# Kernel optimization log

Hardware: AMD Instinct MI355X
Metric: run time of the kernel (lower is better)

## Reference

```python
import jax, jax.numpy as jnp
import numpy as np

NEG_INF = -1e9  # stands in for the eye(W)*sys.maxsize self-mask on the row axis


def setup_inputs() -> dict:
    key = jax.random.key(0)
    ks = jax.random.split(key, 8)
    B, C, S = 8, 512, 128
    C8 = C // 8
    sc = 0.02
    x = jax.random.normal(ks[0], (B, C, S, S), dtype=jnp.float32)
    Wq = jax.random.normal(ks[1], (C8, C), dtype=jnp.float32) * sc
    bq = jnp.zeros((C8,), dtype=jnp.float32)
    Wk = jax.random.normal(ks[2], (C8, C), dtype=jnp.float32) * sc
    bk = jnp.zeros((C8,), dtype=jnp.float32)
    Wv = jax.random.normal(ks[3], (C, C), dtype=jnp.float32) * sc
    bv = jnp.zeros((C,), dtype=jnp.float32)
    gamma = jnp.ones((1,), dtype=jnp.float32) * 0.5  # source inits to 0; nonzero so path is exercised
    return {"x": x, "Wq": Wq, "bq": bq, "Wk": Wk, "bk": bk, "Wv": Wv, "bv": bv, "gamma": gamma}


def reference(x, Wq, bq, Wk, bk, Wv, bv, gamma):
    # x: (B, C, W, H) with W == H == S (required by the eye-mask view in the source)
    B, C, S, _ = x.shape
    # 1x1 convs = per-pixel linear projections
    q = jnp.einsum('oc,bcwh->bowh', Wq, x) + bq[None, :, None, None]  # (B,C8,S,S)
    k = jnp.einsum('oc,bcwh->bowh', Wk, x) + bk[None, :, None, None]
    v = jnp.einsum('oc,bcwh->bowh', Wv, x) + bv[None, :, None, None]  # (B,C,S,S)

    # column ('h'-fixed) attention along W, self position masked out
    e_col = jnp.einsum('bcwh,bcuh->bwhu', q, k)  # (B,W,H,W)
    self_mask = jnp.eye(S, dtype=bool)  # w == u
    e_col = jnp.where(self_mask[None, :, None, :], NEG_INF, e_col)
    # row ('w'-fixed) attention along H
    e_row = jnp.einsum('bcwh,bcwu->bwhu', q, k)  # (B,W,H,H)

    att = jax.nn.softmax(jnp.concatenate([e_col, e_row], axis=-1), axis=-1)  # (B,W,H,2S)
    a_col = att[..., :S]   # weights over w'
    a_row = att[..., S:]   # weights over h'

    out = (jnp.einsum('bwhu,bcuh->bcwh', a_col, v)
           + jnp.einsum('bwhu,bcwu->bcwh', a_row, v))  # (B,C,S,S)
    return gamma[0] * out + x
```

## Files before the change

### kernel.cpp

```cpp
#include <hip/hip_runtime.h>
#include <hip/hip_bf16.h>


#define S 128
#define SS 16384
#define C 512
#define C8 64
#define NEG_BIG -1000000000.0f

using short8 = __attribute__((ext_vector_type(8))) short;
using f32x4  = __attribute__((ext_vector_type(4))) float;

#define GPTR(p) ((const __attribute__((address_space(1))) void*)(p))
#define LPTR(p) ((__attribute__((address_space(3))) void*)(p))

#define PR(r) ((((r) & 7) << 4) | ((r) >> 3))

__device__ __forceinline__ unsigned short f2b(float f){
  union { float f; unsigned u; } v; v.f = f;
  unsigned r = (v.u + 0x7fffu + ((v.u >> 16) & 1u)) >> 16;
  return (unsigned short)r;
}
__device__ __forceinline__ float b2f(unsigned short h){
  union { unsigned u; float f; } v; v.u = ((unsigned)h) << 16;
  return v.f;
}

template<int NT>
__device__ __forceinline__ void stage_tile64(unsigned short* dst,
    const unsigned short* src, size_t rstride, int tid){
  #pragma unroll
  for (int p = 0; p < 1024 / NT; ++p){
    int gi = p * NT + tid;
    int row = gi >> 3, cc = gi & 7;
    int kc = (cc ^ (row & 7)) * 8;
    __builtin_amdgcn_global_load_lds(GPTR(src + (size_t)row * rstride + kc),
                                     LPTR((char*)dst + gi * 16), 16, 0, 0);
  }
}

__global__ __launch_bounds__(256) void k_xp_pack(
    const float* __restrict__ x, unsigned short* __restrict__ xp,
    const float* __restrict__ Wq, const float* __restrict__ Wk,
    const float* __restrict__ Wv, unsigned short* __restrict__ wall){
  __shared__ unsigned short T[128 * 130] __attribute__((aligned(16)));
  int blk = blockIdx.x;
  if (blk >= 4096){
    int i = (blk - 4096) * 256 + threadIdx.x;
    int co = i >> 9, ci = i & (C - 1);
    float v;
    if (co < 64)        v = Wq[co * C + ci];
    else if (co < 128)  v = Wk[(co - 64) * C + ci];
    else                v = Wv[(co - 128) * C + ci];
    wall[i] = f2b(v);
    return;
  }
  int ct = blk & 3; int bw = blk >> 2;
  int w = bw & 127; int b = bw >> 7;
  int tid = threadIdx.x;
  int ci0 = ct * 128;
  const float* xb = x + ((size_t)(b * C + ci0) * S + w) * S;
  #pragma unroll
  for (int p = 0; p < 16; ++p){
    int idx = p * 256 + tid;
    int cc = idx >> 5;
    int h4 = (idx & 31) * 4;
    float4 v = *(const float4*)(xb + (size_t)cc * SS + h4);
    unsigned* d = (unsigned*)&T[PR(cc) * 130 + h4];
    d[0] = (unsigned)f2b(v.x) | ((unsigned)f2b(v.y) << 16);
    d[1] = (unsigned)f2b(v.z) | ((unsigned)f2b(v.w) << 16);
  }
  __syncthreads();
  unsigned short* xpb = xp + (size_t)(b * S + w) * S * C + ci0;
  #pragma unroll
  for (int p = 0; p < 8; ++p){
    int idx = p * 256 + tid;
    int h  = idx >> 4;
    int ch = (idx & 15) * 8;
    unsigned short tmp[8] __attribute__((aligned(16)));
    #pragma unroll
    for (int j = 0; j < 8; ++j) tmp[j] = T[PR(ch + j) * 130 + h];
    *(uint4*)(xpb + (size_t)h * C + ch) = *(uint4*)tmp;
  }
}

__global__ __launch_bounds__(512) void k_qkv(
    const unsigned short* __restrict__ xp, const unsigned short* __restrict__ wall,
    const float* __restrict__ bq, const float* __restrict__ bk,
    const float* __restrict__ bv,
    unsigned short* __restrict__ qp, unsigned short* __restrict__ kp,
    unsigned short* __restrict__ vb){
  __shared__ unsigned short sm[32768] __attribute__((aligned(16)));
  unsigned short* Dl = sm;
  int blk = blockIdx.x;
  int pxsub = blk & 7; int t = blk >> 3;
  int cot = t % 5; int pxg = t / 5;
  int pxt = pxg * 8 + pxsub;
  int w = pxt & 127, b = pxt >> 7;
  int tid = threadIdx.x, lane = tid & 63, wid = tid >> 6;
  int wr = wid & 1, wc = wid >> 1;
  int qd = lane >> 4, ln = lane & 15;
  const unsigned short* asrc0 = wall + (size_t)cot * 128 * C;
  const unsigned short* bsrc0 = xp + (size_t)pxt * 128 * C;
  f32x4 acc[4][2];
  #pragma unroll
  for (int i = 0; i < 4; ++i)
    #pragma unroll
    for (int j = 0; j < 2; ++j) acc[i][j] = (f32x4){0.f, 0.f, 0.f, 0.f};

  stage_tile64<512>(sm,        asrc0, C, tid);
  stage_tile64<512>(sm + 8192, bsrc0, C, tid);
  __syncthreads();

  for (int kw = 0; kw < 8; ++kw){
    unsigned short* Acur = sm + (kw & 1) * 16384;
    unsigned short* Bcur = Acur + 8192;
    if (kw < 7){
      unsigned short* Anxt = sm + ((kw + 1) & 1) * 16384;
      stage_tile64<512>(Anxt,        asrc0 + (kw + 1) * 64, C, tid);
      stage_tile64<512>(Anxt + 8192, bsrc0 + (kw + 1) * 64, C, tid);
    }
    __builtin_amdgcn_s_setprio(1);
    #pragma unroll
    for (int ks = 0; ks < 2; ++ks){
      int ch8 = (((ks * 4 + qd) ^ (ln & 7)) * 8);
      short8 af[4], bfr[2];
      #pragma unroll
      for (int i = 0; i < 4; ++i)
        af[i] = *(const short8*)&Acur[((wr * 4 + i) * 16 + ln) * 64 + ch8];
      #pragma unroll
      for (int j = 0; j < 2; ++j)
        bfr[j] = *(const short8*)&Bcur[((wc * 2 + j) * 16 + ln) * 64 + ch8];
      #pragma unroll
      for (int i = 0; i < 4; ++i)
        #pragma unroll
        for (int j = 0; j < 2; ++j)
          acc[i][j] = __builtin_amdgcn_mfma_f32_16x16x32_bf16(af[i], bfr[j], acc[i][j], 0, 0, 0);
    }
    __builtin_amdgcn_s_setprio(0);
    __syncthreads();
  }
  float bias_[4][4];
  #pragma unroll
  for (int i = 0; i < 4; ++i){
    int co_l0 = (wr * 4 + i) * 16 + qd * 4;
    #pragma unroll
    for (int r = 0; r < 4; ++r){
      int co_l = co_l0 + r;
      bias_[i][r] = (cot == 0) ? (co_l < 64 ? bq[co_l] : bk[co_l - 64])
                               : bv[(cot - 1) * 128 + co_l];
    }
  }
  #pragma unroll
  for (int i = 0; i < 4; ++i){
    int co_l0 = (wr * 4 + i) * 16 + qd * 4;
    #pragma unroll
    for (int j = 0; j < 2; ++j){
      int pxl = (wc * 2 + j) * 16 + ln;
      #pragma unroll
      for (int r = 0; r < 4; ++r)
        Dl[(co_l0 + r) * 136 + pxl] = f2b(acc[i][j][r] + bias_[i][r]);
    }
  }
  __syncthreads();
  if (cot == 0){
    unsigned short* qb = qp + (size_t)(b * S + w) * S * C8;
    unsigned short* kb = kp + (size_t)(b * S + w) * S * C8;
    #pragma unroll
    for (int p = 0; p < 2; ++p){
      int idx = p * 512 + tid;
      int cch = idx & 7, hh = idx >> 3;
      unsigned short tq[8] __attribute__((aligned(16)));
      unsigned short tk[8] __attribute__((aligned(16)));
      #pragma unroll
      for (int jj = 0; jj < 8; ++jj){
        tq[jj] = Dl[(cch * 8 + jj) * 136 + hh];
        tk[jj] = Dl[(64 + cch * 8 + jj) * 136 + hh];
      }
      *(uint4*)(qb + (size_t)hh * C8 + cch * 8) = *(uint4*)tq;
      *(uint4*)(kb + (size_t)hh * C8 + cch * 8) = *(uint4*)tk;
    }
  } else {
    unsigned short* vbb = vb + ((size_t)(b * C + (cot - 1) * 128) * S + w) * S;
    #pragma unroll
    for (int p = 0; p < 4; ++p){
      int idx = p * 512 + tid;
      int c_l = idx >> 4, hc = (idx & 15) * 8;
      uint4 v = *(const uint4*)&Dl[c_l * 136 + hc];
      *(uint4*)(vbb + (size_t)c_l * SS + hc) = v;
    }
  }
}

__global__ __launch_bounds__(256) void k_tv_ecol(
    const unsigned short* __restrict__ vb, unsigned short* __restrict__ vt,
    const unsigned short* __restrict__ qp, const unsigned short* __restrict__ kp,
    unsigned short* __restrict__ eca){
  __shared__ char smu[36864] __attribute__((aligned(16)));
  int blk = blockIdx.x;
  int tid = threadIdx.x;
  if (blk < 4096){
    unsigned short* T = (unsigned short*)smu;
    const unsigned short* src = vb + (size_t)blk * SS;
    unsigned short* dst = vt + (size_t)blk * SS;
    #pragma unroll
    for (int p = 0; p < 8; ++p){
      int idx = p * 256 + tid;
      int wv = idx >> 4, ch = (idx & 15) * 8;
      uint4 v = *(const uint4*)(src + wv * S + ch);
      unsigned* d = (unsigned*)&T[PR(wv) * 130 + ch];
      d[0] = v.x; d[1] = v.y; d[2] = v.z; d[3] = v.w;
    }
    __syncthreads();
    #pragma unroll
    for (int p = 0; p < 8; ++p){
      int idx = p * 256 + tid;
      int h = idx >> 4, ch = (idx & 15) * 8;
      unsigned short tmp[8] __attribute__((aligned(16)));
      #pragma unroll
      for (int j = 0; j < 8; ++j) tmp[j] = T[PR(ch + j) * 130 + h];
      *(uint4*)(dst + h * S + ch) = *(uint4*)tmp;
    }
    return;
  }
  unsigned short* Aq = (unsigned short*)smu;
  unsigned short* Bk = (unsigned short*)(smu + 18432);
  int e = blk - 4096; int h = e & 127, b = e >> 7;
  int lane = tid & 63, wid = tid >> 6;
  int qd = lane >> 4, ln = lane & 15;
  #pragma unroll
  for (int p = 0; p < 4; ++p){
    int idx = p * 256 + tid;
    int row = idx >> 3, ch = (idx & 7) * 8;
    *(uint4*)&Aq[row * 72 + ch] = *(const uint4*)(qp + ((size_t)(b * S + row) * S + h) * C8 + ch);
    *(uint4*)&Bk[row * 72 + ch] = *(const uint4*)(kp + ((size_t)(b * S + row) * S + h) * C8 + ch);
  }
  __syncthreads();
  f32x4 acc[4][4];
  #pragma unroll
  for (int i = 0; i < 4; ++i)
    #pragma unroll
    for (int j = 0; j < 4; ++j) acc[i][j] = (f32x4){0.f, 0.f, 0.f, 0.f};
  #pragma unroll
  for (int ks = 0; ks < 2; ++ks){
    int ko = ks * 32 + qd * 8;
    short8 af[4], bfr[4];
    #pragma unroll
    for (int i = 0; i < 4; ++i)
      af[i] = *(const short8*)&Aq[(((wid & 1) * 4 + i) * 16 + ln) * 72 + ko];
    #pragma unroll
    for (int j = 0; j < 4; ++j)
      bfr[j] = *(const short8*)&Bk[(((wid >> 1) * 4 + j) * 16 + ln) * 72 + ko];
    #pragma unroll
    for (int i = 0; i < 4; ++i)
      #pragma unroll
      for (int j = 0; j < 4; ++j)
        acc[i][j] = __builtin_amdgcn_mfma_f32_16x16x32_bf16(af[i], bfr[j], acc[i][j], 0, 0, 0);
  }
  #pragma unroll
  for (int i = 0; i < 4; ++i){
    int w0 = (((wid & 1) * 4 + i) * 16) + qd * 4;
    #pragma unroll
    for (int j = 0; j < 4; ++j){
      int ug = ((wid >> 1) * 4 + j) * 16 + ln;
      #pragma unroll
      for (int r = 0; r < 4; ++r){
        int wg = w0 + r;
        float val = acc[i][j][r];
        if (wg == ug) val = NEG_BIG;
        eca[((size_t)(b * S + wg) * S + h) * S + ug] = f2b(val);
      }
    }
  }
}

__global__ __launch_bounds__(256) void k_erow_sm_outrow(
    const unsigned short* __restrict__ qp, const unsigned short* __restrict__ kp,
    unsigned short* __restrict__ eca, unsigned short* vb){
  __shared__ char sm[71680] __attribute__((aligned(16)));
  unsigned short* Aq  = (unsigned short*)sm;
  unsigned short* Bk  = (unsigned short*)(sm + 18432);
  unsigned short* El  = (unsigned short*)sm;
  unsigned short* Av0 = (unsigned short*)(sm + 36864);
  unsigned short* Av1 = (unsigned short*)(sm + 53248);
  float* redm = (float*)(sm + 69632);
  float* reds = (float*)(sm + 70656);
  int blk = blockIdx.x; int w = blk & 127, b = blk >> 7;
  int tid = threadIdx.x, lane = tid & 63, wid = tid >> 6;
  int qd = lane >> 4, ln = lane & 15;
  size_t tb = (size_t)(b * S + w) * SS;
  const unsigned short* vsrc0 = vb + (size_t)(b * C) * SS + (size_t)w * S;

  {
    const unsigned short* qsrc = qp + (size_t)(b * S + w) * S * C8;
    const unsigned short* ksrc = kp + (size_t)(b * S + w) * S * C8;
    #pragma unroll
    for (int p = 0; p < 4; ++p){
      int idx = p * 256 + tid;
      int row = idx >> 3, ch = (idx & 7) * 8;
      *(uint4*)&Aq[row * 72 + ch] = *(const uint4*)(qsrc + row * C8 + ch);
      *(uint4*)&Bk[row * 72 + ch] = *(const uint4*)(ksrc + row * C8 + ch);
    }
  }
  stage_tile64<256>(Av0, vsrc0, SS, tid);
  __syncthreads();
  f32x4 acc[4][4];
  #pragma unroll
  for (int i = 0; i < 4; ++i)
    #pragma unroll
    for (int j = 0; j < 4; ++j) acc[i][j] = (f32x4){0.f, 0.f, 0.f, 0.f};
  #pragma unroll
  for (int ks = 0; ks < 2; ++ks){
    int ko = ks * 32 + qd * 8;
    short8 af[4], bfr[4];
    #pragma unroll
    for (int i = 0; i < 4; ++i)
      af[i] = *(const short8*)&Aq[(((wid & 1) * 4 + i) * 16 + ln) * 72 + ko];
    #pragma unroll
    for (int j = 0; j < 4; ++j)
      bfr[j] = *(const short8*)&Bk[(((wid >> 1) * 4 + j) * 16 + ln) * 72 + ko];
    #pragma unroll
    for (int i = 0; i < 4; ++i)
      #pragma unroll
      for (int j = 0; j < 4; ++j)
        acc[i][j] = __builtin_amdgcn_mfma_f32_16x16x32_bf16(af[i], bfr[j], acc[i][j], 0, 0, 0);
  }
  __syncthreads();
  #pragma unroll
  for (int i = 0; i < 4; ++i){
    int h0 = ((wid & 1) * 4 + i) * 16 + qd * 4;
    #pragma unroll
    for (int j = 0; j < 4; ++j){
      int ul = ((wid >> 1) * 4 + j) * 16 + ln;
      #pragma unroll
      for (int r = 0; r < 4; ++r)
        El[(h0 + r) * 136 + ul] = f2b(acc[i][j][r]);
    }
  }
  __syncthreads();
  {
    int h = tid >> 1, half = tid & 1;
    const uint4* src4 = (half == 0) ? (const uint4*)(eca + tb + (size_t)h * S)
                                    : (const uint4*)&El[h * 136];
    float mx = -3.0e38f;
    #pragma unroll 4
    for (int u = 0; u < 16; ++u){
      uint4 v = src4[u];
      const unsigned short* e = (const unsigned short*)&v;
      #pragma unroll
      for (int jj = 0; jj < 8; ++jj) mx = fmaxf(mx, b2f(e[jj]));
    }
    redm[tid] = mx;
    __syncthreads();
    float m = fmaxf(mx, redm[tid ^ 1]);
    float s = 0.f;
    #pragma unroll 4
    for (int u = 0; u < 16; ++u){
      uint4 v = src4[u];
      const unsigned short* e = (const unsigned short*)&v;
      #pragma unroll
      for (int jj = 0; jj < 8; ++jj) s += __expf(b2f(e[jj]) - m);
    }
    reds[tid] = s;
    __syncthreads();
    float inv = 1.0f / (s + reds[tid ^ 1]);
    uint4* dst4 = (half == 0) ? (uint4*)(eca + tb + (size_t)h * S)
                              : (uint4*)&El[h * 136];
    #pragma unroll 4
    for (int u = 0; u < 16; ++u){
      uint4 v = src4[u];
      const unsigned short* e = (const unsigned short*)&v;
      unsigned short o[8] __attribute__((aligned(16)));
      #pragma unroll
      for (int jj = 0; jj < 8; ++jj) o[jj] = f2b(__expf(b2f(e[jj]) - m) * inv);
      dst4[u] = *(uint4*)o;
    }
  }
  __syncthreads();

  for (int s = 0; s < 8; ++s){
    int ct = s >> 1, kw = s & 1;
    unsigned short* Acur = (s & 1) ? Av1 : Av0;
    if (s < 7){
      int ct1 = (s + 1) >> 1, kw1 = (s + 1) & 1;
      stage_tile64<256>((s & 1) ? Av0 : Av1,
                        vsrc0 + (size_t)(ct1 * 128) * SS + kw1 * 64, SS, tid);
    }
    if (kw == 0){
      #pragma unroll
      for (int i = 0; i < 4; ++i)
        #pragma unroll
        for (int j = 0; j < 4; ++j) acc[i][j] = (f32x4){0.f, 0.f, 0.f, 0.f};
    }
    __builtin_amdgcn_s_setprio(1);
    #pragma unroll
    for (int ks = 0; ks < 2; ++ks){
      int ch8 = (((ks * 4 + qd) ^ (ln & 7)) * 8);
      int ko = kw * 64 + ks * 32 + qd * 8;
      short8 af[4], bfr[4];
      #pragma unroll
      for (int i = 0; i < 4; ++i)
        af[i] = *(const short8*)&Acur[(((wid & 1) * 4 + i) * 16 + ln) * 64 + ch8];
      #pragma unroll
      for (int j = 0; j < 4; ++j)
        bfr[j] = *(const short8*)&El[(((wid >> 1) * 4 + j) * 16 + ln) * 136 + ko];
      #pragma unroll
      for (int i = 0; i < 4; ++i)
        #pragma unroll
        for (int j = 0; j < 4; ++j)
          acc[i][j] = __builtin_amdgcn_mfma_f32_16x16x32_bf16(af[i], bfr[j], acc[i][j], 0, 0, 0);
    }
    __builtin_amdgcn_s_setprio(0);
    if (kw == 1){
      #pragma unroll
      for (int i = 0; i < 4; ++i){
        int c0 = ((wid & 1) * 4 + i) * 16 + qd * 4;
        #pragma unroll
        for (int j = 0; j < 4; ++j){
          int hl = ((wid >> 1) * 4 + j) * 16 + ln;
          #pragma unroll
          for (int r = 0; r < 4; ++r){
            int cg = ct * 128 + c0 + r;
            vb[((size_t)(b * C + cg) * S + w) * S + hl] = f2b(acc[i][j][r]);
          }
        }
      }
    }
    __syncthreads();
  }
}

__global__ __launch_bounds__(256) void k_outcol(
    const unsigned short* __restrict__ vt, const unsigned short* __restrict__ eca,
    unsigned short* __restrict__ oct){
  __shared__ unsigned short Av[128 * 72] __attribute__((aligned(16)));
  __shared__ unsigned short Ba[128 * 72] __attribute__((aligned(16)));
  int blk = blockIdx.x;
  int ct = blk & 3; int bh = blk >> 2;
  int h = bh & 127, b = bh >> 7;
  int tid = threadIdx.x, lane = tid & 63, wid = tid >> 6;
  int qd = lane >> 4, ln = lane & 15;
  f32x4 acc[4][4];
  #pragma unroll
  for (int i = 0; i < 4; ++i)
    #pragma unroll
    for (int j = 0; j < 4; ++j) acc[i][j] = (f32x4){0.f, 0.f, 0.f, 0.f};
  for (int kw = 0; kw < 2; ++kw){
    __syncthreads();
    #pragma unroll
    for (int p = 0; p < 4; ++p){
      int idx = p * 256 + tid;
      int row = idx >> 3, ch = (idx & 7) * 8;
      *(uint4*)&Av[row * 72 + ch] =
        *(const uint4*)(vt + ((size_t)(b * C + ct * 128 + row) * S + h) * S + kw * 64 + ch);
      *(uint4*)&Ba[row * 72 + ch] =
        *(const uint4*)(eca + ((size_t)(b * S + row) * S + h) * S + kw * 64 + ch);
    }
    __syncthreads();
    #pragma unroll
    for (int ks = 0; ks < 2; ++ks){
      int ko = ks * 32 + qd * 8;
      short8 af[4], bfr[4];
      #pragma unroll
      for (int i = 0; i < 4; ++i)
        af[i] = *(const short8*)&Av[(((wid & 1) * 4 + i) * 16 + ln) * 72 + ko];
      #pragma unroll
      for (int j = 0; j < 4; ++j)
        bfr[j] = *(const short8*)&Ba[(((wid >> 1) * 4 + j) * 16 + ln) * 72 + ko];
      #pragma unroll
      for (int i = 0; i < 4; ++i)
        #pragma unroll
        for (int j = 0; j < 4; ++j)
          acc[i][j] = __builtin_amdgcn_mfma_f32_16x16x32_bf16(af[i], bfr[j], acc[i][j], 0, 0, 0);
    }
  }
  #pragma unroll
  for (int i = 0; i < 4; ++i){
    int c0 = ((wid & 1) * 4 + i) * 16 + qd * 4;
    #pragma unroll
    for (int j = 0; j < 4; ++j){
      int wl = ((wid >> 1) * 4 + j) * 16 + ln;
      #pragma unroll
      for (int r = 0; r < 4; ++r){
        int cg = ct * 128 + c0 + r;
        oct[((size_t)(b * S + h) * C + cg) * S + wl] = f2b(acc[i][j][r]);
      }
    }
  }
}

__global__ __launch_bounds__(256) void k_final(
    const unsigned short* __restrict__ oct, const unsigned short* __restrict__ orw,
    const float* __restrict__ x, const float* __restrict__ gamma,
    float* __restrict__ out){
  __shared__ unsigned short T[128 * 130] __attribute__((aligned(16)));
  int blk = blockIdx.x;
  int c = blk & 511, b = blk >> 9;
  int tid = threadIdx.x;
  float g = gamma[0];
  #pragma unroll
  for (int p = 0; p < 8; ++p){
    int idx = p * 256 + tid;
    int hh = idx >> 4, ch = (idx & 15) * 8;
    uint4 v = *(const uint4*)(oct + ((size_t)(b * S + hh) * C + c) * S + ch);
    unsigned* d = (unsigned*)&T[PR(hh) * 130 + ch];
    d[0] = v.x; d[1] = v.y; d[2] = v.z; d[3] = v.w;
  }
  __syncthreads();
  #pragma unroll
  for (int p = 0; p < 8; ++p){
    int idx = p * 256 + tid;
    int wv = idx >> 4, hch = (idx & 15) * 8;
    size_t o = ((size_t)(b * C + c) * S + wv) * S + hch;
    uint4 rv = *(const uint4*)(orw + o);
    const unsigned short* rr = (const unsigned short*)&rv;
    float4 x0 = *(const float4*)(x + o);
    float4 x1 = *(const float4*)(x + o + 4);
    float4 o0, o1;
    o0.x = g * (b2f(rr[0]) + b2f(T[PR(hch + 0) * 130 + wv])) + x0.x;
    o0.y = g * (b2f(rr[1]) + b2f(T[PR(hch + 1) * 130 + wv])) + x0.y;
    o0.z = g * (b2f(rr[2]) + b2f(T[PR(hch + 2) * 130 + wv])) + x0.z;
    o0.w = g * (b2f(rr[3]) + b2f(T[PR(hch + 3) * 130 + wv])) + x0.w;
    o1.x = g * (b2f(rr[4]) + b2f(T[PR(hch + 4) * 130 + wv])) + x1.x;
    o1.y = g * (b2f(rr[5]) + b2f(T[PR(hch + 5) * 130 + wv])) + x1.y;
    o1.z = g * (b2f(rr[6]) + b2f(T[PR(hch + 6) * 130 + wv])) + x1.z;
    o1.w = g * (b2f(rr[7]) + b2f(T[PR(hch + 7) * 130 + wv])) + x1.w;
    *(float4*)(out + o) = o0;
    *(float4*)(out + o + 4) = o1;
  }
}

extern "C" void kernel_launch(void* const* d_in, const int* in_sizes, int n_in,
                              void* d_out, int out_size, void* d_ws, size_t ws_size,
                              hipStream_t stream){
  const float* x     = (const float*)d_in[0];
  const float* Wq    = (const float*)d_in[1];
  const float* bq    = (const float*)d_in[2];
  const float* Wk    = (const float*)d_in[3];
  const float* bk    = (const float*)d_in[4];
  const float* Wv    = (const float*)d_in[5];
  const float* bv    = (const float*)d_in[6];
  const float* gamma = (const float*)d_in[7];
  float* out = (float*)d_out;
  char* ws = (char*)d_ws;

  const size_t OFF_WALL = 0;
  const size_t OFF_XP   = 1ull << 20;
  const size_t OFF_QP   = OFF_XP  + 134217728ull;
  const size_t OFF_KP   = OFF_QP  + 16777216ull;
  const size_t OFF_VB   = OFF_KP  + 16777216ull;
  const size_t OFF_VT   = OFF_VB  + 134217728ull;
  const size_t OFF_ECA  = OFF_VT  + 134217728ull;
  const size_t OFF_OCT  = OFF_XP;
  const size_t NEED     = OFF_ECA + 33554432ull;
  if (ws_size < NEED) return;

  unsigned short* wall = (unsigned short*)(ws + OFF_WALL);
  unsigned short* xp   = (unsigned short*)(ws + OFF_XP);
  unsigned short* qp   = (unsigned short*)(ws + OFF_QP);
  unsigned short* kp   = (unsigned short*)(ws + OFF_KP);
  unsigned short* vb   = (unsigned short*)(ws + OFF_VB);
  unsigned short* vt   = (unsigned short*)(ws + OFF_VT);
  unsigned short* eca  = (unsigned short*)(ws + OFF_ECA);
  unsigned short* oct  = (unsigned short*)(ws + OFF_OCT);

  k_xp_pack       <<<5376, 256, 0, stream>>>(x, xp, Wq, Wk, Wv, wall);
  k_qkv           <<<5120, 512, 0, stream>>>(xp, wall, bq, bk, bv, qp, kp, vb);
  k_tv_ecol       <<<5120, 256, 0, stream>>>(vb, vt, qp, kp, eca);
  k_erow_sm_outrow<<<1024, 256, 0, stream>>>(qp, kp, eca, vb);
  k_outcol        <<<4096, 256, 0, stream>>>(vt, eca, oct);
  k_final         <<<4096, 256, 0, stream>>>(oct, vb, x, gamma, out);
}
```

Measured before the change: 917.3 us.

## Restructure QKV GEMM: weights in registers, triple-buffered LDS for activations

The QKV projection kernel drops from 512 to 256 threads per block, with each wave computing a 4x4 MFMA tile instead of 4x2. Weight fragments are now loaded from global memory directly into double-buffered registers, so only the activation tile goes through shared memory. That tile uses a three-slot LDS ring with prefetch two steps ahead, and explicit vmcnt waits plus a raw barrier replace the per-iteration __syncthreads. The aim is to cut LDS traffic and barrier stalls and to overlap loads with MFMA work. The cost is higher register pressure and fragile hand-counted waitcnt values.

Measured after the change: 990.2 us. +7.9%, slower.

```diff
diff --git a/kernel.cpp b/kernel.cpp
--- a/kernel.cpp
+++ b/kernel.cpp
@@ -84,13 +84,13 @@
   }
 }
 
-__global__ __launch_bounds__(512) void k_qkv(
+__global__ __launch_bounds__(256) void k_qkv(
     const unsigned short* __restrict__ xp, const unsigned short* __restrict__ wall,
     const float* __restrict__ bq, const float* __restrict__ bk,
     const float* __restrict__ bv,
     unsigned short* __restrict__ qp, unsigned short* __restrict__ kp,
     unsigned short* __restrict__ vb){
-  __shared__ unsigned short sm[32768] __attribute__((aligned(16)));
+  __shared__ unsigned short sm[24576] __attribute__((aligned(16)));
   unsigned short* Dl = sm;
   int blk = blockIdx.x;
   int pxsub = blk & 7; int t = blk >> 3;
@@ -98,52 +98,66 @@
   int pxt = pxg * 8 + pxsub;
   int w = pxt & 127, b = pxt >> 7;
   int tid = threadIdx.x, lane = tid & 63, wid = tid >> 6;
-  int wr = wid & 1, wc = wid >> 1;
   int qd = lane >> 4, ln = lane & 15;
   const unsigned short* asrc0 = wall + (size_t)cot * 128 * C;
   const unsigned short* bsrc0 = xp + (size_t)pxt * 128 * C;
-  f32x4 acc[4][2];
+  const unsigned short* arow[4];
   #pragma unroll
   for (int i = 0; i < 4; ++i)
-    #pragma unroll
-    for (int j = 0; j < 2; ++j) acc[i][j] = (f32x4){0.f, 0.f, 0.f, 0.f};
-
-  stage_tile64<512>(sm,        asrc0, C, tid);
-  stage_tile64<512>(sm + 8192, bsrc0, C, tid);
-  __syncthreads();
-
+    arow[i] = asrc0 + (size_t)(((wid & 1) * 4 + i) * 16 + ln) * C + qd * 8;
+  f32x4 acc[4][4];
+  #pragma unroll
+  for (int i = 0; i < 4; ++i)
+    #pragma unroll
+    for (int j = 0; j < 4; ++j) acc[i][j] = (f32x4){0.f, 0.f, 0.f, 0.f};
+  short8 afr[2][2][4];
+
+  stage_tile64<256>(sm,        bsrc0,      C, tid);
+  stage_tile64<256>(sm + 8192, bsrc0 + 64, C, tid);
+  #pragma unroll
+  for (int ks = 0; ks < 2; ++ks)
+    #pragma unroll
+    for (int i = 0; i < 4; ++i)
+      afr[0][ks][i] = *(const short8*)(arow[i] + ks * 32);
+
+  #pragma unroll
   for (int kw = 0; kw < 8; ++kw){
-    unsigned short* Acur = sm + (kw & 1) * 16384;
-    unsigned short* Bcur = Acur + 8192;
+    if (kw < 7) asm volatile("s_waitcnt vmcnt(12)" ::: "memory");
+    else        asm volatile("s_waitcnt vmcnt(0)"  ::: "memory");
+    __builtin_amdgcn_s_barrier();
     if (kw < 7){
-      unsigned short* Anxt = sm + ((kw + 1) & 1) * 16384;
-      stage_tile64<512>(Anxt,        asrc0 + (kw + 1) * 64, C, tid);
-      stage_tile64<512>(Anxt + 8192, bsrc0 + (kw + 1) * 64, C, tid);
-    }
+      #pragma unroll
+      for (int ks = 0; ks < 2; ++ks)
+        #pragma unroll
+        for (int i = 0; i < 4; ++i)
+          afr[(kw + 1) & 1][ks][i] =
+            *(const short8*)(arow[i] + (kw + 1) * 64 + ks * 32);
+    }
+    if (kw < 6)
+      stage_tile64<256>(sm + ((kw + 2) % 3) * 8192,
+                        bsrc0 + (kw + 2) * 64, C, tid);
+    const unsigned short* Bl = sm + (kw % 3) * 8192;
     __builtin_amdgcn_s_setprio(1);
     #pragma unroll
     for (int ks = 0; ks < 2; ++ks){
       int ch8 = (((ks * 4 + qd) ^ (ln & 7)) * 8);
-      short8 af[4], bfr[2];
-      #pragma unroll
-      for (int i = 0; i < 4; ++i)
-        af[i] = *(const short8*)&Acur[((wr * 4 + i) * 16 + ln) * 64 + ch8];
-      #pragma unroll
-      for (int j = 0; j < 2; ++j)
-        bfr[j] = *(const short8*)&Bcur[((wc * 2 + j) * 16 + ln) * 64 + ch8];
+      short8 bfr[4];
+      #pragma unroll
+      for (int j = 0; j < 4; ++j)
+        bfr[j] = *(const short8*)&Bl[(((wid >> 1) * 4 + j) * 16 + ln) * 64 + ch8];
       #pragma unroll
       for (int i = 0; i < 4; ++i)
         #pragma unroll
-        for (int j = 0; j < 2; ++j)
-          acc[i][j] = __builtin_amdgcn_mfma_f32_16x16x32_bf16(af[i], bfr[j], acc[i][j], 0, 0, 0);
+        for (int j = 0; j < 4; ++j)
+          acc[i][j] = __builtin_amdgcn_mfma_f32_16x16x32_bf16(afr[kw & 1][ks][i], bfr[j], acc[i][j], 0, 0, 0);
     }
     __builtin_amdgcn_s_setprio(0);
-    __syncthreads();
-  }
+  }
+  __syncthreads();
   float bias_[4][4];
   #pragma unroll
   for (int i = 0; i < 4; ++i){
-    int co_l0 = (wr * 4 + i) * 16 + qd * 4;
+    int co_l0 = ((wid & 1) * 4 + i) * 16 + qd * 4;
     #pragma unroll
     for (int r = 0; r < 4; ++r){
       int co_l = co_l0 + r;
@@ -153,10 +167,10 @@
   }
   #pragma unroll
   for (int i = 0; i < 4; ++i){
-    int co_l0 = (wr * 4 + i) * 16 + qd * 4;
-    #pragma unroll
-    for (int j = 0; j < 2; ++j){
-      int pxl = (wc * 2 + j) * 16 + ln;
+    int co_l0 = ((wid & 1) * 4 + i) * 16 + qd * 4;
+    #pragma unroll
+    for (int j = 0; j < 4; ++j){
+      int pxl = ((wid >> 1) * 4 + j) * 16 + ln;
       #pragma unroll
       for (int r = 0; r < 4; ++r)
         Dl[(co_l0 + r) * 136 + pxl] = f2b(acc[i][j][r] + bias_[i][r]);
@@ -167,8 +181,8 @@
     unsigned short* qb = qp + (size_t)(b * S + w) * S * C8;
     unsigned short* kb = kp + (size_t)(b * S + w) * S * C8;
     #pragma unroll
-    for (int p = 0; p < 2; ++p){
-      int idx = p * 512 + tid;
+    for (int p = 0; p < 4; ++p){
+      int idx = p * 256 + tid;
       int cch = idx & 7, hh = idx >> 3;
       unsigned short tq[8] __attribute__((aligned(16)));
       unsigned short tk[8] __attribute__((aligned(16)));
@@ -183,8 +197,8 @@
   } else {
     unsigned short* vbb = vb + ((size_t)(b * C + (cot - 1) * 128) * S + w) * S;
     #pragma unroll
-    for (int p = 0; p < 4; ++p){
-      int idx = p * 512 + tid;
+    for (int p = 0; p < 8; ++p){
+      int idx = p * 256 + tid;
       int c_l = idx >> 4, hc = (idx & 15) * 8;
       uint4 v = *(const uint4*)&Dl[c_l * 136 + hc];
       *(uint4*)(vbb + (size_t)c_l * SS + hc) = v;
@@ -565,7 +579,7 @@
   unsigned short* oct  = (unsigned short*)(ws + OFF_OCT);
 
   k_xp_pack       <<<5376, 256, 0, stream>>>(x, xp, Wq, Wk, Wv, wall);
-  k_qkv           <<<5120, 512, 0, stream>>>(xp, wall, bq, bk, bv, qp, kp, vb);
+  k_qkv           <<<5120, 256, 0, stream>>>(xp, wall, bq, bk, bv, qp, kp, vb);
   k_tv_ecol       <<<5120, 256, 0, stream>>>(vb, vt, qp, kp, eca);
   k_erow_sm_outrow<<<1024, 256, 0, stream>>>(qp, kp, eca, vb);
   k_outcol        <<<4096, 256, 0, stream>>>(vt, eca, oct);
```
